# Kernel optimization log

Hardware: AMD Instinct MI355X
Metric: run time of the kernel (lower is better)

## Reference

```python
import jax, jax.numpy as jnp
import numpy as np

N = 50000
IN_C, HID_C, OUT_C = 128, 64, 32
E = 800000
NEG_SLOPE = 0.2


def setup_inputs() -> dict:
    key = jax.random.key(0)
    ks = jax.random.split(key, 8)
    x = jax.random.normal(ks[0], (N, IN_C), dtype=jnp.float32)
    edge_index = jax.random.randint(ks[1], (2, E), 0, N, dtype=jnp.int64)
    # GATConv params (heads=1): lin weight, att_src/att_dst vectors, bias
    sc = 1.0 / np.sqrt(IN_C)
    W = jax.random.uniform(ks[2], (IN_C, HID_C), jnp.float32, -sc, sc)
    att_src = jax.random.normal(ks[3], (HID_C,), jnp.float32) * (1.0 / np.sqrt(HID_C))
    att_dst = jax.random.normal(ks[4], (HID_C,), jnp.float32) * (1.0 / np.sqrt(HID_C))
    bias_conv = jnp.zeros((HID_C,), jnp.float32)
    sl = 1.0 / np.sqrt(HID_C)
    W_lin = jax.random.uniform(ks[5], (HID_C, OUT_C), jnp.float32, -sl, sl)
    b_lin = jax.random.uniform(ks[6], (OUT_C,), jnp.float32, -sl, sl)
    return {"x": x, "edge_index": edge_index, "W": W, "att_src": att_src,
            "att_dst": att_dst, "bias_conv": bias_conv, "W_lin": W_lin, "b_lin": b_lin}


def reference(x, edge_index, W, att_src, att_dst, bias_conv, W_lin, b_lin):
    n = x.shape[0]
    h = x @ W  # [N, HID]
    # add self-loops (PyG GATConv default add_self_loops=True)
    loop = jnp.arange(n, dtype=edge_index.dtype)
    src = jnp.concatenate([edge_index[0], loop])  # [E+N]
    dst = jnp.concatenate([edge_index[1], loop])
    a_src = h @ att_src  # [N]
    a_dst = h @ att_dst
    e = jax.nn.leaky_relu(a_src[src] + a_dst[dst], NEG_SLOPE)  # [E+N]
    # segment softmax over incoming edges per destination node
    m = jax.ops.segment_max(e, dst, num_segments=n)
    e = jnp.exp(e - m[dst])
    denom = jax.ops.segment_sum(e, dst, num_segments=n)
    alpha = e / (denom[dst] + 1e-16)
    msg = alpha[:, None] * h[src]  # [E+N, HID]
    out = jax.ops.segment_sum(msg, dst, num_segments=n) + bias_conv
    out = jax.nn.relu(out)
    return out @ W_lin + b_lin
```

## Files before the change

kernel.cpp:

```cpp
#include <hip/hip_runtime.h>
#include <hip/hip_bf16.h>

#define IN_C  128
#define HID_C 64
#define OUT_C 32
#define NEG_SLOPE 0.2f
#define EPB     2048
#define BUCKETW 64
#define RCAP    1536
#define SUPW    1024
#define RCAP1   18432
#define PARTS   9
#define CSTRIDE 16
#define XS_LD   136

typedef short bf16x8 __attribute__((ext_vector_type(8)));
typedef float f32x4  __attribute__((ext_vector_type(4)));

__device__ __forceinline__ unsigned short f2bf(float f) {
    __hip_bfloat16 h = __float2bfloat16(f);
    return *(unsigned short*)&h;
}
__device__ __forceinline__ float bflo(unsigned int u) {
    return __uint_as_float(u << 16);
}
__device__ __forceinline__ float bfhi(unsigned int u) {
    return __uint_as_float(u & 0xffff0000u);
}

__global__ __launch_bounds__(256) void gemm_mfma_kernel(
    const float* __restrict__ x, const float* __restrict__ W,
    const float* __restrict__ att_src, const float* __restrict__ att_dst,
    __hip_bfloat16* __restrict__ hb,
    float* __restrict__ a_src, float* __restrict__ a_dst,
    int* __restrict__ bcursor, int ncur, int n_nodes)
{
    __shared__ unsigned short xs[16 * XS_LD];
    __shared__ float redA[4][16];
    __shared__ float redD[4][16];
    const int t    = threadIdx.x;
    const int wv   = t >> 6;
    const int lane = t & 63;
    const int m16  = lane & 15;
    const int quad = lane >> 4;
    const int node0 = blockIdx.x * 16;
    const int nrows = min(16, n_nodes - node0);

    const int gid = blockIdx.x * 256 + t;
    if (gid < ncur) bcursor[gid] = 0;

    const int ncol = wv * 16 + m16;
    bf16x8 B[4];
#pragma unroll
    for (int k0 = 0; k0 < 4; ++k0)
#pragma unroll
        for (int j = 0; j < 8; ++j)
            B[k0][j] = (short)f2bf(W[(k0 * 32 + quad * 8 + j) * HID_C + ncol]);

    {
        const float4* xg = (const float4*)(x + (long)node0 * IN_C);
#pragma unroll
        for (int i = t; i < 512; i += 256) {
            const int row = i >> 5;
            const int c4  = i & 31;
            float4 v = (row < nrows) ? xg[i] : make_float4(0.f, 0.f, 0.f, 0.f);
            ushort4 u;
            u.x = f2bf(v.x); u.y = f2bf(v.y);
            u.z = f2bf(v.z); u.w = f2bf(v.w);
            *(ushort4*)(xs + row * XS_LD + c4 * 4) = u;
        }
    }
    __syncthreads();

    f32x4 C = {0.f, 0.f, 0.f, 0.f};
#pragma unroll
    for (int k0 = 0; k0 < 4; ++k0) {
        const bf16x8 A = *(const bf16x8*)(xs + m16 * XS_LD + k0 * 32 + quad * 8);
        C = __builtin_amdgcn_mfma_f32_16x16x32_bf16(A, B[k0], C, 0, 0, 0);
    }

#pragma unroll
    for (int r = 0; r < 4; ++r) {
        const int row = quad * 4 + r;
        if (row < nrows)
            hb[(long)(node0 + row) * HID_C + ncol] = __float2bfloat16(C[r]);
    }

    {
        const float av = att_src[ncol];
        const float dv = att_dst[ncol];
        float ps[4], pd[4];
#pragma unroll
        for (int r = 0; r < 4; ++r) { ps[r] = C[r] * av; pd[r] = C[r] * dv; }
#pragma unroll
        for (int off = 1; off <= 8; off <<= 1) {
#pragma unroll
            for (int r = 0; r < 4; ++r) {
                ps[r] += __shfl_xor(ps[r], off, 64);
                pd[r] += __shfl_xor(pd[r], off, 64);
            }
        }
        if (m16 == 0) {
#pragma unroll
            for (int r = 0; r < 4; ++r) {
                redA[wv][quad * 4 + r] = ps[r];
                redD[wv][quad * 4 + r] = pd[r];
            }
        }
    }
    __syncthreads();
    if (t < 16 && t < nrows) {
        a_src[node0 + t] = redA[0][t] + redA[1][t] + redA[2][t] + redA[3][t];
        a_dst[node0 + t] = redD[0][t] + redD[1][t] + redD[2][t] + redD[3][t];
    }
}

__global__ __launch_bounds__(256) void bin1_kernel(
    const int* __restrict__ ei, int E,
    const float* __restrict__ a_src, const float* __restrict__ a_dst,
    int* __restrict__ bcur1, uint2* __restrict__ superbuf)
{
    __shared__ uint2 stage[EPB];
    __shared__ int excl[64];
    __shared__ int cur[64];
    __shared__ int gpos[64];

    const int t = threadIdx.x;
    const int base = blockIdx.x * EPB;
    const int nedge = min(EPB, E - base);

    if (t < 64) excl[t] = 0;
    __syncthreads();

    for (int i = t; i < nedge; i += 256)
        atomicAdd(&excl[ei[E + base + i] >> 10], 1);
    __syncthreads();

    if (t < 64) {
        int c = excl[t], incl = c;
#pragma unroll
        for (int off = 1; off <= 32; off <<= 1) {
            int u = __shfl_up(incl, off, 64);
            if (t >= off) incl += u;
        }
        excl[t] = incl - c;
        cur[t]  = incl - c;
    }
    __syncthreads();

    for (int i = t; i < nedge; i += 256) {
        const int s = ei[base + i];
        const int d = ei[E + base + i];
        float e = a_src[s] + a_dst[d];
        e = (e >= 0.f) ? e : NEG_SLOPE * e;
        const float w = __expf(e);
        const int sq = d >> 10;
        const int pos = atomicAdd(&cur[sq], 1);
        stage[pos] = make_uint2((unsigned)s | ((unsigned)(d & 1023) << 16)
                                | ((unsigned)sq << 26),
                                __float_as_uint(w));
    }
    __syncthreads();

    if (t < 64) {
        const int c = cur[t] - excl[t];
        gpos[t] = (c > 0) ? atomicAdd(&bcur1[t * CSTRIDE], c) : 0;
    }
    __syncthreads();

    for (int i = t; i < nedge; i += 256) {
        const uint2 r = stage[i];
        const int sq = r.x >> 26;
        const int dp = gpos[sq] + (i - excl[sq]);
        if (dp < RCAP1) superbuf[(long)sq * RCAP1 + dp] = r;
    }
}

__global__ __launch_bounds__(256) void bin2_kernel(
    const uint2* __restrict__ superbuf, const int* __restrict__ bcur1,
    int* __restrict__ bcur2, uint2* __restrict__ bucketbuf)
{
    __shared__ uint2 srt[EPB];
    __shared__ int cnt[16];
    __shared__ int rp[16];
    __shared__ int cur16[16];
    __shared__ int gpos[16];

    const int t    = threadIdx.x;
    const int sq   = blockIdx.x / PARTS;
    const int part = blockIdx.x % PARTS;
    const int tot  = min(bcur1[sq * CSTRIDE], RCAP1);
    const int beg  = part * EPB;
    const int n    = min(EPB, tot - beg);
    if (n <= 0) return;

    if (t < 16) cnt[t] = 0;
    __syncthreads();

    const uint2* src = superbuf + (long)sq * RCAP1 + beg;

    for (int i = t; i < n; i += 256)
        atomicAdd(&cnt[(src[i].x >> 22) & 15], 1);
    __syncthreads();

    if (t == 0) {
        int run = 0;
#pragma unroll
        for (int k = 0; k < 16; ++k) { rp[k] = run; cur16[k] = run; run += cnt[k]; }
    }
    __syncthreads();

    for (int i = t; i < n; i += 256) {
        const uint2 r = src[i];
        const int pos = atomicAdd(&cur16[(r.x >> 22) & 15], 1);
        srt[pos] = r;
    }
    __syncthreads();

    if (t < 16) {
        const int c = cnt[t];
        const int q2 = sq * 16 + t;
        gpos[t] = (c > 0) ? atomicAdd(&bcur2[q2 * CSTRIDE], c) : 0;
    }
    __syncthreads();

    for (int i = t; i < n; i += 256) {
        const uint2 r = srt[i];
        const int idx = (r.x >> 22) & 15;
        const int dp  = gpos[idx] + (i - rp[idx]);
        const int q2  = sq * 16 + idx;
        const unsigned nx = (r.x & 0xFFFFu) | (((r.x >> 16) & 63u) << 16);
        if (dp < RCAP) bucketbuf[(long)q2 * RCAP + dp] = make_uint2(nx, r.y);
    }
}

__global__ __launch_bounds__(512) void bucket_agg_kernel(
    const uint2* __restrict__ bucketbuf, const int* __restrict__ bcursor,
    const __hip_bfloat16* __restrict__ hb,
    const float* __restrict__ a_src, const float* __restrict__ a_dst,
    const float* __restrict__ bias_conv,
    const float* __restrict__ W_lin, const float* __restrict__ b_lin,
    float* __restrict__ out, int n_nodes)
{
    __shared__ uint2 srtL[RCAP];
    __shared__ int cntd[BUCKETW];
    __shared__ int rp[BUCKETW + 1];
    __shared__ int curd[BUCKETW];

    const int t  = threadIdx.x;
    const int q  = blockIdx.x;
    const int d0 = q * BUCKETW;
    const int dmax = min(BUCKETW, n_nodes - d0);
    const int tot  = min(bcursor[q * CSTRIDE], RCAP);
    const int wv = t >> 6, lane = t & 63, g8 = lane >> 3, l = lane & 7;

    if (t < BUCKETW) cntd[t] = 0;
    __syncthreads();

    const uint2* gsrc = bucketbuf + (long)q * RCAP;

    for (int i = t; i < tot; i += 512)
        atomicAdd(&cntd[(gsrc[i].x >> 16) & 63], 1);
    __syncthreads();

    if (t < 64) {
        int c = cntd[t], incl = c;
#pragma unroll
        for (int off = 1; off <= 32; off <<= 1) {
            int u = __shfl_up(incl, off, 64);
            if (t >= off) incl += u;
        }
        rp[t] = incl - c;
        curd[t] = incl - c;
        if (t == 63) rp[64] = incl;
    }
    __syncthreads();

    for (int i = t; i < tot; i += 512) {
        const uint2 r = gsrc[i];
        const int pos = atomicAdd(&curd[(r.x >> 16) & 63], 1);
        srtL[pos] = r;
    }
    __syncthreads();

    float Wr[8][4];
#pragma unroll
    for (int kc = 0; kc < 8; ++kc)
#pragma unroll
        for (int kj = 0; kj < 4; ++kj)
            Wr[kc][kj] = W_lin[(l * 8 + kc) * OUT_C + g8 * 4 + kj];
    float biasR[8];
#pragma unroll
    for (int kc = 0; kc < 8; ++kc) biasR[kc] = bias_conv[l * 8 + kc];
    float blinR[4];
#pragma unroll
    for (int kj = 0; kj < 4; ++kj) blinR[kj] = b_lin[g8 * 4 + kj];

    const unsigned short* hbs = (const unsigned short*)hb;

    for (int dloc = wv; dloc < dmax; dloc += 8) {
        const int d = d0 + dloc;
        float A[8] = {0.f,0.f,0.f,0.f,0.f,0.f,0.f,0.f};
        float den = 0.f;
        if (g8 == 0) {
            float e = a_src[d] + a_dst[d];
            e = (e >= 0.f) ? e : NEG_SLOPE * e;
            const float ws = __expf(e);
            const uint4 hv = *(const uint4*)(hbs + (long)d * HID_C + l * 8);
            den = ws;
            A[0] = ws * bflo(hv.x); A[1] = ws * bfhi(hv.x);
            A[2] = ws * bflo(hv.y); A[3] = ws * bfhi(hv.y);
            A[4] = ws * bflo(hv.z); A[5] = ws * bfhi(hv.z);
            A[6] = ws * bflo(hv.w); A[7] = ws * bfhi(hv.w);
        }
        const int beg = rp[dloc], fin = rp[dloc + 1];
        for (int j = beg + g8; j < fin; j += 16) {
            const int  j1   = j + 8;
            const bool has1 = j1 < fin;
            const uint2 r0 = srtL[j];
            const uint2 r1 = srtL[has1 ? j1 : j];
            const int   s0 = r0.x & 0xFFFF;
            const int   s1 = r1.x & 0xFFFF;
            const float w0 = __uint_as_float(r0.y);
            const float w1 = has1 ? __uint_as_float(r1.y) : 0.f;
            const uint4 h0 = *(const uint4*)(hbs + (long)s0 * HID_C + l * 8);
            const uint4 h1 = *(const uint4*)(hbs + (long)s1 * HID_C + l * 8);
            den += w0 + w1;
            A[0] = fmaf(w0, bflo(h0.x), A[0]); A[1] = fmaf(w0, bfhi(h0.x), A[1]);
            A[2] = fmaf(w0, bflo(h0.y), A[2]); A[3] = fmaf(w0, bfhi(h0.y), A[3]);
            A[4] = fmaf(w0, bflo(h0.z), A[4]); A[5] = fmaf(w0, bfhi(h0.z), A[5]);
            A[6] = fmaf(w0, bflo(h0.w), A[6]); A[7] = fmaf(w0, bfhi(h0.w), A[7]);
            A[0] = fmaf(w1, bflo(h1.x), A[0]); A[1] = fmaf(w1, bfhi(h1.x), A[1]);
            A[2] = fmaf(w1, bflo(h1.y), A[2]); A[3] = fmaf(w1, bfhi(h1.y), A[3]);
            A[4] = fmaf(w1, bflo(h1.z), A[4]); A[5] = fmaf(w1, bfhi(h1.z), A[5]);
            A[6] = fmaf(w1, bflo(h1.w), A[6]); A[7] = fmaf(w1, bfhi(h1.w), A[7]);
        }
#pragma unroll
        for (int off = 8; off <= 32; off <<= 1) {
#pragma unroll
            for (int k = 0; k < 8; ++k) A[k] += __shfl_xor(A[k], off, 64);
            den += __shfl_xor(den, off, 64);
        }
        const float rd = 1.0f / (den + 1e-16f);
        float p0 = 0.f, p1 = 0.f, p2 = 0.f, p3 = 0.f;
#pragma unroll
        for (int kc = 0; kc < 8; ++kc) {
            float vv = fmaf(A[kc], rd, biasR[kc]);
            vv = vv > 0.f ? vv : 0.f;
            p0 = fmaf(vv, Wr[kc][0], p0);
            p1 = fmaf(vv, Wr[kc][1], p1);
            p2 = fmaf(vv, Wr[kc][2], p2);
            p3 = fmaf(vv, Wr[kc][3], p3);
        }
#pragma unroll
        for (int off = 1; off <= 4; off <<= 1) {
            p0 += __shfl_xor(p0, off, 64);
            p1 += __shfl_xor(p1, off, 64);
            p2 += __shfl_xor(p2, off, 64);
            p3 += __shfl_xor(p3, off, 64);
        }
        if (l == 0) {
            float4 o = make_float4(p0 + blinR[0], p1 + blinR[1],
                                   p2 + blinR[2], p3 + blinR[3]);
            *(float4*)(out + (long)d * OUT_C + g8 * 4) = o;
        }
    }
}

extern "C" void kernel_launch(void* const* d_in, const int* in_sizes, int n_in,
                              void* d_out, int out_size, void* d_ws, size_t ws_size,
                              hipStream_t stream) {
    const float* x         = (const float*)d_in[0];
    const int*   ei        = (const int*)d_in[1];
    const float* W         = (const float*)d_in[2];
    const float* att_src   = (const float*)d_in[3];
    const float* att_dst   = (const float*)d_in[4];
    const float* bias_conv = (const float*)d_in[5];
    const float* W_lin     = (const float*)d_in[6];
    const float* b_lin     = (const float*)d_in[7];
    float*       out       = (float*)d_out;

    const int n_nodes = in_sizes[0] / IN_C;
    const int E       = in_sizes[1] / 2;
    const int B    = (E + EPB - 1) / EPB;
    const int Q    = (n_nodes + BUCKETW - 1) / BUCKETW;
    const int NSUP = (n_nodes + SUPW - 1) / SUPW;

    __hip_bfloat16* hb = (__hip_bfloat16*)d_ws;
    float* a_src   = (float*)(hb + (long)n_nodes * HID_C);
    float* a_dst   = a_src + n_nodes;
    int*   bcur1   = (int*)(a_dst + n_nodes);
    int*   bcur2   = bcur1 + NSUP * CSTRIDE;
    uint2* superbuf  = (uint2*)(bcur2 + (long)Q * CSTRIDE);
    uint2* bucketbuf = superbuf + (long)NSUP * RCAP1;

    const int ncur = (NSUP + Q) * CSTRIDE;

    gemm_mfma_kernel<<<(n_nodes + 15) / 16, 256, 0, stream>>>(
        x, W, att_src, att_dst, hb, a_src, a_dst,
        bcur1, ncur, n_nodes);

    bin1_kernel<<<B, 256, 0, stream>>>(
        ei, E, a_src, a_dst, bcur1, superbuf);

    bin2_kernel<<<NSUP * PARTS, 256, 0, stream>>>(
        superbuf, bcur1, bcur2, bucketbuf);

    bucket_agg_kernel<<<Q, 512, 0, stream>>>(
        bucketbuf, bcur2, hb, a_src, a_dst,
        bias_conv, W_lin, b_lin, out, n_nodes);
}
```

Before: 163.8 us.

## Make GEMM persistent per-wave with register-resident W; shrink bin1 edge chunk

The projection GEMM becomes a grid-stride loop in which each wave keeps the whole bf16 W slice in registers. Each wave computes a full 16x64 tile straight from global x, with no LDS staging and no cross-wave reduction. This removes the per-block reload and conversion of W across thousands of tiny blocks. The bin1 edge chunk per block is halved so more blocks run in parallel. The cost is much higher register pressure, and the row bounds check is dropped, so the code assumes the node count is a multiple of 16.

```diff
diff --git a/kernel.cpp b/kernel.cpp
--- a/kernel.cpp
+++ b/kernel.cpp
@@ -5,14 +5,14 @@
 #define HID_C 64
 #define OUT_C 32
 #define NEG_SLOPE 0.2f
-#define EPB     2048
+#define EPB1    1024
+#define EPB2    2048
 #define BUCKETW 64
 #define RCAP    1536
 #define SUPW    1024
 #define RCAP1   18432
 #define PARTS   9
 #define CSTRIDE 16
-#define XS_LD   136
 
 typedef short bf16x8 __attribute__((ext_vector_type(8)));
 typedef float f32x4  __attribute__((ext_vector_type(4)));
@@ -28,70 +28,81 @@
     return __uint_as_float(u & 0xffff0000u);
 }
 
-__global__ __launch_bounds__(256) void gemm_mfma_kernel(
+__global__ __launch_bounds__(256, 2) void gemm_mfma_kernel(
     const float* __restrict__ x, const float* __restrict__ W,
     const float* __restrict__ att_src, const float* __restrict__ att_dst,
     __hip_bfloat16* __restrict__ hb,
     float* __restrict__ a_src, float* __restrict__ a_dst,
-    int* __restrict__ bcursor, int ncur, int n_nodes)
+    int* __restrict__ bcursor, int ncur, int ntiles)
 {
-    __shared__ unsigned short xs[16 * XS_LD];
-    __shared__ float redA[4][16];
-    __shared__ float redD[4][16];
     const int t    = threadIdx.x;
-    const int wv   = t >> 6;
+    const int gid  = blockIdx.x * 256 + t;
     const int lane = t & 63;
     const int m16  = lane & 15;
     const int quad = lane >> 4;
-    const int node0 = blockIdx.x * 16;
-    const int nrows = min(16, n_nodes - node0);
-
-    const int gid = blockIdx.x * 256 + t;
+    const int gwave  = gid >> 6;
+    const int nwaves = (gridDim.x * 256) >> 6;
+
     if (gid < ncur) bcursor[gid] = 0;
 
-    const int ncol = wv * 16 + m16;
-    bf16x8 B[4];
-#pragma unroll
-    for (int k0 = 0; k0 < 4; ++k0)
-#pragma unroll
-        for (int j = 0; j < 8; ++j)
-            B[k0][j] = (short)f2bf(W[(k0 * 32 + quad * 8 + j) * HID_C + ncol]);
-
-    {
-        const float4* xg = (const float4*)(x + (long)node0 * IN_C);
-#pragma unroll
-        for (int i = t; i < 512; i += 256) {
-            const int row = i >> 5;
-            const int c4  = i & 31;
-            float4 v = (row < nrows) ? xg[i] : make_float4(0.f, 0.f, 0.f, 0.f);
-            ushort4 u;
-            u.x = f2bf(v.x); u.y = f2bf(v.y);
-            u.z = f2bf(v.z); u.w = f2bf(v.w);
-            *(ushort4*)(xs + row * XS_LD + c4 * 4) = u;
-        }
-    }
-    __syncthreads();
-
-    f32x4 C = {0.f, 0.f, 0.f, 0.f};
-#pragma unroll
-    for (int k0 = 0; k0 < 4; ++k0) {
-        const bf16x8 A = *(const bf16x8*)(xs + m16 * XS_LD + k0 * 32 + quad * 8);
-        C = __builtin_amdgcn_mfma_f32_16x16x32_bf16(A, B[k0], C, 0, 0, 0);
-    }
-
-#pragma unroll
-    for (int r = 0; r < 4; ++r) {
-        const int row = quad * 4 + r;
-        if (row < nrows)
-            hb[(long)(node0 + row) * HID_C + ncol] = __float2bfloat16(C[r]);
-    }
-
-    {
-        const float av = att_src[ncol];
-        const float dv = att_dst[ncol];
-        float ps[4], pd[4];
-#pragma unroll
-        for (int r = 0; r < 4; ++r) { ps[r] = C[r] * av; pd[r] = C[r] * dv; }
+    bf16x8 B[4][4];
+#pragma unroll
+    for (int ct = 0; ct < 4; ++ct)
+#pragma unroll
+        for (int k0 = 0; k0 < 4; ++k0)
+#pragma unroll
+            for (int j = 0; j < 8; ++j)
+                B[ct][k0][j] = (short)f2bf(
+                    W[(k0 * 32 + quad * 8 + j) * HID_C + ct * 16 + m16]);
+
+    float attS[4], attD[4];
+#pragma unroll
+    for (int ct = 0; ct < 4; ++ct) {
+        attS[ct] = att_src[ct * 16 + m16];
+        attD[ct] = att_dst[ct * 16 + m16];
+    }
+
+    for (int tile = gwave; tile < ntiles; tile += nwaves) {
+        const int node0 = tile * 16;
+        const float* xr = x + (long)(node0 + m16) * IN_C + quad * 8;
+
+        bf16x8 A[4];
+#pragma unroll
+        for (int k0 = 0; k0 < 4; ++k0) {
+            const float4 v0 = *(const float4*)(xr + k0 * 32);
+            const float4 v1 = *(const float4*)(xr + k0 * 32 + 4);
+            A[k0][0] = (short)f2bf(v0.x); A[k0][1] = (short)f2bf(v0.y);
+            A[k0][2] = (short)f2bf(v0.z); A[k0][3] = (short)f2bf(v0.w);
+            A[k0][4] = (short)f2bf(v1.x); A[k0][5] = (short)f2bf(v1.y);
+            A[k0][6] = (short)f2bf(v1.z); A[k0][7] = (short)f2bf(v1.w);
+        }
+
+        f32x4 C[4];
+#pragma unroll
+        for (int ct = 0; ct < 4; ++ct) {
+            C[ct] = (f32x4){0.f, 0.f, 0.f, 0.f};
+#pragma unroll
+            for (int k0 = 0; k0 < 4; ++k0)
+                C[ct] = __builtin_amdgcn_mfma_f32_16x16x32_bf16(
+                    A[k0], B[ct][k0], C[ct], 0, 0, 0);
+        }
+
+#pragma unroll
+        for (int ct = 0; ct < 4; ++ct)
+#pragma unroll
+            for (int r = 0; r < 4; ++r)
+                hb[(long)(node0 + quad * 4 + r) * HID_C + ct * 16 + m16] =
+                    __float2bfloat16(C[ct][r]);
+
+        float ps[4] = {0.f, 0.f, 0.f, 0.f};
+        float pd[4] = {0.f, 0.f, 0.f, 0.f};
+#pragma unroll
+        for (int ct = 0; ct < 4; ++ct)
+#pragma unroll
+            for (int r = 0; r < 4; ++r) {
+                ps[r] = fmaf(C[ct][r], attS[ct], ps[r]);
+                pd[r] = fmaf(C[ct][r], attD[ct], pd[r]);
+            }
 #pragma unroll
         for (int off = 1; off <= 8; off <<= 1) {
 #pragma unroll
@@ -103,15 +114,10 @@
         if (m16 == 0) {
 #pragma unroll
             for (int r = 0; r < 4; ++r) {
-                redA[wv][quad * 4 + r] = ps[r];
-                redD[wv][quad * 4 + r] = pd[r];
+                a_src[node0 + quad * 4 + r] = ps[r];
+                a_dst[node0 + quad * 4 + r] = pd[r];
             }
         }
-    }
-    __syncthreads();
-    if (t < 16 && t < nrows) {
-        a_src[node0 + t] = redA[0][t] + redA[1][t] + redA[2][t] + redA[3][t];
-        a_dst[node0 + t] = redD[0][t] + redD[1][t] + redD[2][t] + redD[3][t];
     }
 }
 
@@ -120,14 +126,14 @@
     const float* __restrict__ a_src, const float* __restrict__ a_dst,
     int* __restrict__ bcur1, uint2* __restrict__ superbuf)
 {
-    __shared__ uint2 stage[EPB];
+    __shared__ uint2 stage[EPB1];
     __shared__ int excl[64];
     __shared__ int cur[64];
     __shared__ int gpos[64];
 
     const int t = threadIdx.x;
-    const int base = blockIdx.x * EPB;
-    const int nedge = min(EPB, E - base);
+    const int base = blockIdx.x * EPB1;
+    const int nedge = min(EPB1, E - base);
 
     if (t < 64) excl[t] = 0;
     __syncthreads();
@@ -180,7 +186,7 @@
     const uint2* __restrict__ superbuf, const int* __restrict__ bcur1,
     int* __restrict__ bcur2, uint2* __restrict__ bucketbuf)
 {
-    __shared__ uint2 srt[EPB];
+    __shared__ uint2 srt[EPB2];
     __shared__ int cnt[16];
     __shared__ int rp[16];
     __shared__ int cur16[16];
@@ -190,8 +196,8 @@
     const int sq   = blockIdx.x / PARTS;
     const int part = blockIdx.x % PARTS;
     const int tot  = min(bcur1[sq * CSTRIDE], RCAP1);
-    const int beg  = part * EPB;
-    const int n    = min(EPB, tot - beg);
+    const int beg  = part * EPB2;
+    const int n    = min(EPB2, tot - beg);
     if (n <= 0) return;
 
     if (t < 16) cnt[t] = 0;
@@ -382,9 +388,10 @@
 
     const int n_nodes = in_sizes[0] / IN_C;
     const int E       = in_sizes[1] / 2;
-    const int B    = (E + EPB - 1) / EPB;
+    const int B1   = (E + EPB1 - 1) / EPB1;
     const int Q    = (n_nodes + BUCKETW - 1) / BUCKETW;
     const int NSUP = (n_nodes + SUPW - 1) / SUPW;
+    const int ntiles = (n_nodes + 15) / 16;
 
     __hip_bfloat16* hb = (__hip_bfloat16*)d_ws;
     float* a_src   = (float*)(hb + (long)n_nodes * HID_C);
@@ -396,11 +403,11 @@
 
     const int ncur = (NSUP + Q) * CSTRIDE;
 
-    gemm_mfma_kernel<<<(n_nodes + 15) / 16, 256, 0, stream>>>(
+    gemm_mfma_kernel<<<512, 256, 0, stream>>>(
         x, W, att_src, att_dst, hb, a_src, a_dst,
-        bcur1, ncur, n_nodes);
-
-    bin1_kernel<<<B, 256, 0, stream>>>(
+        bcur1, ncur, ntiles);
+
+    bin1_kernel<<<B1, 256, 0, stream>>>(
         ei, E, a_src, a_dst, bcur1, superbuf);
 
     bin2_kernel<<<NSUP * PARTS, 256, 0, stream>>>(
```

After: 168.2 us. 1.03x slower.

## Split aggregation across two channel-half blocks per bucket with atomic output accumulation

Applied to the files above, without the earlier changes.

Launches two blocks per destination bucket in the aggregation kernel, each handling 32 of the 64 hidden channels. Each block computes a partial output projection and accumulates it into the output with atomicAdd. The output is zeroed inside the GEMM kernel, and only the first half adds b_lin. This doubles the grid for more parallelism and halves per-thread registers. In exchange, both blocks redo the counting sort of the bucket's edges, the softmax denominator is computed twice, and there is atomic traffic on the output.

```diff
diff --git a/kernel.cpp b/kernel.cpp
--- a/kernel.cpp
+++ b/kernel.cpp
@@ -5,7 +5,8 @@
 #define HID_C 64
 #define OUT_C 32
 #define NEG_SLOPE 0.2f
-#define EPB     2048
+#define EPB1    2048
+#define EPB2    2048
 #define BUCKETW 64
 #define RCAP    1536
 #define SUPW    1024
@@ -33,7 +34,8 @@
     const float* __restrict__ att_src, const float* __restrict__ att_dst,
     __hip_bfloat16* __restrict__ hb,
     float* __restrict__ a_src, float* __restrict__ a_dst,
-    int* __restrict__ bcursor, int ncur, int n_nodes)
+    int* __restrict__ bcursor, int ncur,
+    float* __restrict__ outz, int nout2, int n_nodes)
 {
     __shared__ unsigned short xs[16 * XS_LD];
     __shared__ float redA[4][16];
@@ -48,6 +50,7 @@
 
     const int gid = blockIdx.x * 256 + t;
     if (gid < ncur) bcursor[gid] = 0;
+    if (gid < nout2) ((float2*)outz)[gid] = make_float2(0.f, 0.f);
 
     const int ncol = wv * 16 + m16;
     bf16x8 B[4];
@@ -120,14 +123,14 @@
     const float* __restrict__ a_src, const float* __restrict__ a_dst,
     int* __restrict__ bcur1, uint2* __restrict__ superbuf)
 {
-    __shared__ uint2 stage[EPB];
+    __shared__ uint2 stage[EPB1];
     __shared__ int excl[64];
     __shared__ int cur[64];
     __shared__ int gpos[64];
 
     const int t = threadIdx.x;
-    const int base = blockIdx.x * EPB;
-    const int nedge = min(EPB, E - base);
+    const int base = blockIdx.x * EPB1;
+    const int nedge = min(EPB1, E - base);
 
     if (t < 64) excl[t] = 0;
     __syncthreads();
@@ -180,7 +183,7 @@
     const uint2* __restrict__ superbuf, const int* __restrict__ bcur1,
     int* __restrict__ bcur2, uint2* __restrict__ bucketbuf)
 {
-    __shared__ uint2 srt[EPB];
+    __shared__ uint2 srt[EPB2];
     __shared__ int cnt[16];
     __shared__ int rp[16];
     __shared__ int cur16[16];
@@ -190,8 +193,8 @@
     const int sq   = blockIdx.x / PARTS;
     const int part = blockIdx.x % PARTS;
     const int tot  = min(bcur1[sq * CSTRIDE], RCAP1);
-    const int beg  = part * EPB;
-    const int n    = min(EPB, tot - beg);
+    const int beg  = part * EPB2;
+    const int n    = min(EPB2, tot - beg);
     if (n <= 0) return;
 
     if (t < 16) cnt[t] = 0;
@@ -248,11 +251,13 @@
     __shared__ int curd[BUCKETW];
 
     const int t  = threadIdx.x;
-    const int q  = blockIdx.x;
+    const int q  = blockIdx.x >> 1;
+    const int ch = blockIdx.x & 1;
     const int d0 = q * BUCKETW;
     const int dmax = min(BUCKETW, n_nodes - d0);
     const int tot  = min(bcursor[q * CSTRIDE], RCAP);
     const int wv = t >> 6, lane = t & 63, g8 = lane >> 3, l = lane & 7;
+    const int cbase = ch * 32 + l * 4;
 
     if (t < BUCKETW) cntd[t] = 0;
     __syncthreads();
@@ -283,35 +288,34 @@
     }
     __syncthreads();
 
-    float Wr[8][4];
-#pragma unroll
-    for (int kc = 0; kc < 8; ++kc)
+    float Wr[4][4];
+#pragma unroll
+    for (int kc = 0; kc < 4; ++kc)
 #pragma unroll
         for (int kj = 0; kj < 4; ++kj)
-            Wr[kc][kj] = W_lin[(l * 8 + kc) * OUT_C + g8 * 4 + kj];
-    float biasR[8];
-#pragma unroll
-    for (int kc = 0; kc < 8; ++kc) biasR[kc] = bias_conv[l * 8 + kc];
+            Wr[kc][kj] = W_lin[(cbase + kc) * OUT_C + g8 * 4 + kj];
+    float biasR[4];
+#pragma unroll
+    for (int kc = 0; kc < 4; ++kc) biasR[kc] = bias_conv[cbase + kc];
     float blinR[4];
 #pragma unroll
-    for (int kj = 0; kj < 4; ++kj) blinR[kj] = b_lin[g8 * 4 + kj];
+    for (int kj = 0; kj < 4; ++kj)
+        blinR[kj] = (ch == 0) ? b_lin[g8 * 4 + kj] : 0.f;
 
     const unsigned short* hbs = (const unsigned short*)hb;
 
     for (int dloc = wv; dloc < dmax; dloc += 8) {
         const int d = d0 + dloc;
-        float A[8] = {0.f,0.f,0.f,0.f,0.f,0.f,0.f,0.f};
+        float A[4] = {0.f, 0.f, 0.f, 0.f};
         float den = 0.f;
         if (g8 == 0) {
             float e = a_src[d] + a_dst[d];
             e = (e >= 0.f) ? e : NEG_SLOPE * e;
             const float ws = __expf(e);
-            const uint4 hv = *(const uint4*)(hbs + (long)d * HID_C + l * 8);
+            const uint2 hv = *(const uint2*)(hbs + (long)d * HID_C + cbase);
             den = ws;
             A[0] = ws * bflo(hv.x); A[1] = ws * bfhi(hv.x);
             A[2] = ws * bflo(hv.y); A[3] = ws * bfhi(hv.y);
-            A[4] = ws * bflo(hv.z); A[5] = ws * bfhi(hv.z);
-            A[6] = ws * bflo(hv.w); A[7] = ws * bfhi(hv.w);
         }
         const int beg = rp[dloc], fin = rp[dloc + 1];
         for (int j = beg + g8; j < fin; j += 16) {
@@ -323,28 +327,24 @@
             const int   s1 = r1.x & 0xFFFF;
             const float w0 = __uint_as_float(r0.y);
             const float w1 = has1 ? __uint_as_float(r1.y) : 0.f;
-            const uint4 h0 = *(const uint4*)(hbs + (long)s0 * HID_C + l * 8);
-            const uint4 h1 = *(const uint4*)(hbs + (long)s1 * HID_C + l * 8);
+            const uint2 h0 = *(const uint2*)(hbs + (long)s0 * HID_C + cbase);
+            const uint2 h1 = *(const uint2*)(hbs + (long)s1 * HID_C + cbase);
             den += w0 + w1;
             A[0] = fmaf(w0, bflo(h0.x), A[0]); A[1] = fmaf(w0, bfhi(h0.x), A[1]);
             A[2] = fmaf(w0, bflo(h0.y), A[2]); A[3] = fmaf(w0, bfhi(h0.y), A[3]);
-            A[4] = fmaf(w0, bflo(h0.z), A[4]); A[5] = fmaf(w0, bfhi(h0.z), A[5]);
-            A[6] = fmaf(w0, bflo(h0.w), A[6]); A[7] = fmaf(w0, bfhi(h0.w), A[7]);
             A[0] = fmaf(w1, bflo(h1.x), A[0]); A[1] = fmaf(w1, bfhi(h1.x), A[1]);
             A[2] = fmaf(w1, bflo(h1.y), A[2]); A[3] = fmaf(w1, bfhi(h1.y), A[3]);
-            A[4] = fmaf(w1, bflo(h1.z), A[4]); A[5] = fmaf(w1, bfhi(h1.z), A[5]);
-            A[6] = fmaf(w1, bflo(h1.w), A[6]); A[7] = fmaf(w1, bfhi(h1.w), A[7]);
         }
 #pragma unroll
         for (int off = 8; off <= 32; off <<= 1) {
 #pragma unroll
-            for (int k = 0; k < 8; ++k) A[k] += __shfl_xor(A[k], off, 64);
+            for (int k = 0; k < 4; ++k) A[k] += __shfl_xor(A[k], off, 64);
             den += __shfl_xor(den, off, 64);
         }
         const float rd = 1.0f / (den + 1e-16f);
         float p0 = 0.f, p1 = 0.f, p2 = 0.f, p3 = 0.f;
 #pragma unroll
-        for (int kc = 0; kc < 8; ++kc) {
+        for (int kc = 0; kc < 4; ++kc) {
             float vv = fmaf(A[kc], rd, biasR[kc]);
             vv = vv > 0.f ? vv : 0.f;
             p0 = fmaf(vv, Wr[kc][0], p0);
@@ -360,9 +360,11 @@
             p3 += __shfl_xor(p3, off, 64);
         }
         if (l == 0) {
-            float4 o = make_float4(p0 + blinR[0], p1 + blinR[1],
-                                   p2 + blinR[2], p3 + blinR[3]);
-            *(float4*)(out + (long)d * OUT_C + g8 * 4) = o;
+            float* op = out + (long)d * OUT_C + g8 * 4;
+            atomicAdd(op + 0, p0 + blinR[0]);
+            atomicAdd(op + 1, p1 + blinR[1]);
+            atomicAdd(op + 2, p2 + blinR[2]);
+            atomicAdd(op + 3, p3 + blinR[3]);
         }
     }
 }
@@ -382,7 +384,7 @@
 
     const int n_nodes = in_sizes[0] / IN_C;
     const int E       = in_sizes[1] / 2;
-    const int B    = (E + EPB - 1) / EPB;
+    const int B1   = (E + EPB1 - 1) / EPB1;
     const int Q    = (n_nodes + BUCKETW - 1) / BUCKETW;
     const int NSUP = (n_nodes + SUPW - 1) / SUPW;
 
@@ -394,19 +396,20 @@
     uint2* superbuf  = (uint2*)(bcur2 + (long)Q * CSTRIDE);
     uint2* bucketbuf = superbuf + (long)NSUP * RCAP1;
 
-    const int ncur = (NSUP + Q) * CSTRIDE;
+    const int ncur  = (NSUP + Q) * CSTRIDE;
+    const int nout2 = n_nodes * OUT_C / 2;
 
     gemm_mfma_kernel<<<(n_nodes + 15) / 16, 256, 0, stream>>>(
         x, W, att_src, att_dst, hb, a_src, a_dst,
-        bcur1, ncur, n_nodes);
-
-    bin1_kernel<<<B, 256, 0, stream>>>(
+        bcur1, ncur, out, nout2, n_nodes);
+
+    bin1_kernel<<<B1, 256, 0, stream>>>(
         ei, E, a_src, a_dst, bcur1, superbuf);
 
     bin2_kernel<<<NSUP * PARTS, 256, 0, stream>>>(
         superbuf, bcur1, bcur2, bucketbuf);
 
-    bucket_agg_kernel<<<Q, 512, 0, stream>>>(
+    bucket_agg_kernel<<<Q * 2, 512, 0, stream>>>(
         bucketbuf, bcur2, hb, a_src, a_dst,
         bias_conv, W_lin, b_lin, out, n_nodes);
 }
```

After: 179.7 us. 1.1x slower.

## Defer edge weight computation to aggregation, halve binned edge record size

Applied to the files above, without the earlier changes.

The binning kernels no longer gather a_src/a_dst or compute exp weights. They move 4-byte packed index records instead of 8-byte records, which halves traffic through superbuf, bucketbuf and shared memory. The aggregation kernel now gathers a_src[s] per edge and recomputes the leaky-relu and exp. That adds a random gather and transcendental work to the hot loop, but removes two random gathers and a wide store from bin1.

```diff
diff --git a/kernel.cpp b/kernel.cpp
--- a/kernel.cpp
+++ b/kernel.cpp
@@ -5,7 +5,8 @@
 #define HID_C 64
 #define OUT_C 32
 #define NEG_SLOPE 0.2f
-#define EPB     2048
+#define EPB1    2048
+#define EPB2    2048
 #define BUCKETW 64
 #define RCAP    1536
 #define SUPW    1024
@@ -117,17 +118,16 @@
 
 __global__ __launch_bounds__(256) void bin1_kernel(
     const int* __restrict__ ei, int E,
-    const float* __restrict__ a_src, const float* __restrict__ a_dst,
-    int* __restrict__ bcur1, uint2* __restrict__ superbuf)
+    int* __restrict__ bcur1, unsigned* __restrict__ superbuf)
 {
-    __shared__ uint2 stage[EPB];
+    __shared__ unsigned stage[EPB1];
     __shared__ int excl[64];
     __shared__ int cur[64];
     __shared__ int gpos[64];
 
     const int t = threadIdx.x;
-    const int base = blockIdx.x * EPB;
-    const int nedge = min(EPB, E - base);
+    const int base = blockIdx.x * EPB1;
+    const int nedge = min(EPB1, E - base);
 
     if (t < 64) excl[t] = 0;
     __syncthreads();
@@ -151,14 +151,10 @@
     for (int i = t; i < nedge; i += 256) {
         const int s = ei[base + i];
         const int d = ei[E + base + i];
-        float e = a_src[s] + a_dst[d];
-        e = (e >= 0.f) ? e : NEG_SLOPE * e;
-        const float w = __expf(e);
         const int sq = d >> 10;
         const int pos = atomicAdd(&cur[sq], 1);
-        stage[pos] = make_uint2((unsigned)s | ((unsigned)(d & 1023) << 16)
-                                | ((unsigned)sq << 26),
-                                __float_as_uint(w));
+        stage[pos] = (unsigned)s | ((unsigned)(d & 1023) << 16)
+                     | ((unsigned)sq << 26);
     }
     __syncthreads();
 
@@ -169,18 +165,18 @@
     __syncthreads();
 
     for (int i = t; i < nedge; i += 256) {
-        const uint2 r = stage[i];
-        const int sq = r.x >> 26;
+        const unsigned r = stage[i];
+        const int sq = r >> 26;
         const int dp = gpos[sq] + (i - excl[sq]);
         if (dp < RCAP1) superbuf[(long)sq * RCAP1 + dp] = r;
     }
 }
 
 __global__ __launch_bounds__(256) void bin2_kernel(
-    const uint2* __restrict__ superbuf, const int* __restrict__ bcur1,
-    int* __restrict__ bcur2, uint2* __restrict__ bucketbuf)
+    const unsigned* __restrict__ superbuf, const int* __restrict__ bcur1,
+    int* __restrict__ bcur2, unsigned* __restrict__ bucketbuf)
 {
-    __shared__ uint2 srt[EPB];
+    __shared__ unsigned srt[EPB2];
     __shared__ int cnt[16];
     __shared__ int rp[16];
     __shared__ int cur16[16];
@@ -190,17 +186,17 @@
     const int sq   = blockIdx.x / PARTS;
     const int part = blockIdx.x % PARTS;
     const int tot  = min(bcur1[sq * CSTRIDE], RCAP1);
-    const int beg  = part * EPB;
-    const int n    = min(EPB, tot - beg);
+    const int beg  = part * EPB2;
+    const int n    = min(EPB2, tot - beg);
     if (n <= 0) return;
 
     if (t < 16) cnt[t] = 0;
     __syncthreads();
 
-    const uint2* src = superbuf + (long)sq * RCAP1 + beg;
+    const unsigned* src = superbuf + (long)sq * RCAP1 + beg;
 
     for (int i = t; i < n; i += 256)
-        atomicAdd(&cnt[(src[i].x >> 22) & 15], 1);
+        atomicAdd(&cnt[(src[i] >> 22) & 15], 1);
     __syncthreads();
 
     if (t == 0) {
@@ -211,8 +207,8 @@
     __syncthreads();
 
     for (int i = t; i < n; i += 256) {
-        const uint2 r = src[i];
-        const int pos = atomicAdd(&cur16[(r.x >> 22) & 15], 1);
+        const unsigned r = src[i];
+        const int pos = atomicAdd(&cur16[(r >> 22) & 15], 1);
         srt[pos] = r;
     }
     __syncthreads();
@@ -225,24 +221,24 @@
     __syncthreads();
 
     for (int i = t; i < n; i += 256) {
-        const uint2 r = srt[i];
-        const int idx = (r.x >> 22) & 15;
+        const unsigned r = srt[i];
+        const int idx = (r >> 22) & 15;
         const int dp  = gpos[idx] + (i - rp[idx]);
         const int q2  = sq * 16 + idx;
-        const unsigned nx = (r.x & 0xFFFFu) | (((r.x >> 16) & 63u) << 16);
-        if (dp < RCAP) bucketbuf[(long)q2 * RCAP + dp] = make_uint2(nx, r.y);
+        const unsigned nx = (r & 0xFFFFu) | (((r >> 16) & 63u) << 16);
+        if (dp < RCAP) bucketbuf[(long)q2 * RCAP + dp] = nx;
     }
 }
 
 __global__ __launch_bounds__(512) void bucket_agg_kernel(
-    const uint2* __restrict__ bucketbuf, const int* __restrict__ bcursor,
+    const unsigned* __restrict__ bucketbuf, const int* __restrict__ bcursor,
     const __hip_bfloat16* __restrict__ hb,
     const float* __restrict__ a_src, const float* __restrict__ a_dst,
     const float* __restrict__ bias_conv,
     const float* __restrict__ W_lin, const float* __restrict__ b_lin,
     float* __restrict__ out, int n_nodes)
 {
-    __shared__ uint2 srtL[RCAP];
+    __shared__ unsigned srtL[RCAP];
     __shared__ int cntd[BUCKETW];
     __shared__ int rp[BUCKETW + 1];
     __shared__ int curd[BUCKETW];
@@ -257,10 +253,10 @@
     if (t < BUCKETW) cntd[t] = 0;
     __syncthreads();
 
-    const uint2* gsrc = bucketbuf + (long)q * RCAP;
+    const unsigned* gsrc = bucketbuf + (long)q * RCAP;
 
     for (int i = t; i < tot; i += 512)
-        atomicAdd(&cntd[(gsrc[i].x >> 16) & 63], 1);
+        atomicAdd(&cntd[(gsrc[i] >> 16) & 63], 1);
     __syncthreads();
 
     if (t < 64) {
@@ -277,8 +273,8 @@
     __syncthreads();
 
     for (int i = t; i < tot; i += 512) {
-        const uint2 r = gsrc[i];
-        const int pos = atomicAdd(&curd[(r.x >> 16) & 63], 1);
+        const unsigned r = gsrc[i];
+        const int pos = atomicAdd(&curd[(r >> 16) & 63], 1);
         srtL[pos] = r;
     }
     __syncthreads();
@@ -300,10 +296,11 @@
 
     for (int dloc = wv; dloc < dmax; dloc += 8) {
         const int d = d0 + dloc;
+        const float ad = a_dst[d];
         float A[8] = {0.f,0.f,0.f,0.f,0.f,0.f,0.f,0.f};
         float den = 0.f;
         if (g8 == 0) {
-            float e = a_src[d] + a_dst[d];
+            float e = a_src[d] + ad;
             e = (e >= 0.f) ? e : NEG_SLOPE * e;
             const float ws = __expf(e);
             const uint4 hv = *(const uint4*)(hbs + (long)d * HID_C + l * 8);
@@ -317,14 +314,18 @@
         for (int j = beg + g8; j < fin; j += 16) {
             const int  j1   = j + 8;
             const bool has1 = j1 < fin;
-            const uint2 r0 = srtL[j];
-            const uint2 r1 = srtL[has1 ? j1 : j];
-            const int   s0 = r0.x & 0xFFFF;
-            const int   s1 = r1.x & 0xFFFF;
-            const float w0 = __uint_as_float(r0.y);
-            const float w1 = has1 ? __uint_as_float(r1.y) : 0.f;
+            const unsigned r0 = srtL[j];
+            const unsigned r1 = srtL[has1 ? j1 : j];
+            const int   s0 = r0 & 0xFFFF;
+            const int   s1 = r1 & 0xFFFF;
+            const float as0 = a_src[s0];
+            const float as1 = a_src[s1];
             const uint4 h0 = *(const uint4*)(hbs + (long)s0 * HID_C + l * 8);
             const uint4 h1 = *(const uint4*)(hbs + (long)s1 * HID_C + l * 8);
+            float e0 = as0 + ad; e0 = (e0 >= 0.f) ? e0 : NEG_SLOPE * e0;
+            float e1 = as1 + ad; e1 = (e1 >= 0.f) ? e1 : NEG_SLOPE * e1;
+            const float w0 = __expf(e0);
+            const float w1 = has1 ? __expf(e1) : 0.f;
             den += w0 + w1;
             A[0] = fmaf(w0, bflo(h0.x), A[0]); A[1] = fmaf(w0, bfhi(h0.x), A[1]);
             A[2] = fmaf(w0, bflo(h0.y), A[2]); A[3] = fmaf(w0, bfhi(h0.y), A[3]);
@@ -382,7 +383,7 @@
 
     const int n_nodes = in_sizes[0] / IN_C;
     const int E       = in_sizes[1] / 2;
-    const int B    = (E + EPB - 1) / EPB;
+    const int B1   = (E + EPB1 - 1) / EPB1;
     const int Q    = (n_nodes + BUCKETW - 1) / BUCKETW;
     const int NSUP = (n_nodes + SUPW - 1) / SUPW;
 
@@ -391,8 +392,8 @@
     float* a_dst   = a_src + n_nodes;
     int*   bcur1   = (int*)(a_dst + n_nodes);
     int*   bcur2   = bcur1 + NSUP * CSTRIDE;
-    uint2* superbuf  = (uint2*)(bcur2 + (long)Q * CSTRIDE);
-    uint2* bucketbuf = superbuf + (long)NSUP * RCAP1;
+    unsigned* superbuf  = (unsigned*)(bcur2 + (long)Q * CSTRIDE);
+    unsigned* bucketbuf = superbuf + (long)NSUP * RCAP1;
 
     const int ncur = (NSUP + Q) * CSTRIDE;
 
@@ -400,8 +401,7 @@
         x, W, att_src, att_dst, hb, a_src, a_dst,
         bcur1, ncur, n_nodes);
 
-    bin1_kernel<<<B, 256, 0, stream>>>(
-        ei, E, a_src, a_dst, bcur1, superbuf);
+    bin1_kernel<<<B1, 256, 0, stream>>>(ei, E, bcur1, superbuf);
 
     bin2_kernel<<<NSUP * PARTS, 256, 0, stream>>>(
         superbuf, bcur1, bcur2, bucketbuf);
```

Result: faster. 158.6 us (-3.1%).
